# Kernel optimization log

Measured on AMD Instinct MI355X. Metric: run time of the kernel, lower is better.

The kernel has to match this reference:

```python
import jax, jax.numpy as jnp
import numpy as np

H = 8                 # num_heads
SCALE = 25.0          # self.scale
SIM_THRESH = 0.75
CONF_SIM_THRESH = 0.99


def _l2n(x):
    return x / jnp.linalg.norm(x, axis=-1, keepdims=True)


def setup_inputs() -> dict:
    key = jax.random.key(0)
    ks = jax.random.split(key, 10)
    B, N1, N2, C = 1, 512, 2048, 1024
    s = 0.02
    return {
        'x_cls': jax.random.normal(ks[0], (B, N2, C), jnp.float32),
        'x_reg': jax.random.normal(ks[1], (B, N2, C), jnp.float32),
        'cls_score': jax.random.uniform(ks[2], (N2,), dtype=jnp.float32),
        'fg_score': jax.random.uniform(ks[3], (N2,), dtype=jnp.float32),
        'W_q_cls': jax.random.normal(ks[4], (C, C), jnp.float32) * s,
        'W_kv_cls': jax.random.normal(ks[5], (C, 2 * C), jnp.float32) * s,
        'W_q_reg': jax.random.normal(ks[6], (C, C), jnp.float32) * s,
        'W_kv_reg': jax.random.normal(ks[7], (C, 2 * C), jnp.float32) * s,
        'W_lin': jax.random.normal(ks[8], (2 * C, 2 * C), jnp.float32) * s,
        'b_lin': jnp.zeros((2 * C,), jnp.float32),
        'W_lin_reg': jax.random.normal(ks[9], (2 * C, 2 * C), jnp.float32) * s,
        'b_lin_reg': jnp.zeros((2 * C,), jnp.float32),
        'local_preds_num': 512,
    }


def _forward(x_cls, x_reg, cls_score, fg_score, W_q_cls, W_kv_cls, W_q_reg, W_kv_reg,
             W_lin, b_lin, W_lin_reg, b_lin_reg, N1):
    B, N2, C = x_cls.shape
    hd = C // H
    # QKV projections (torch Linear with bias=False; weights stored [in,out])
    q_cls = (x_cls[:, :N1] @ W_q_cls).reshape(B, N1, H, hd).transpose(0, 2, 1, 3)   # [B,H,N1,hd]
    kv = (x_cls @ W_kv_cls).reshape(B, N2, 2, H, hd).transpose(2, 0, 3, 1, 4)
    k_cls, v_cls = kv[0], kv[1]                                                      # [B,H,N2,hd]
    q_reg = (x_reg[:, :N1] @ W_q_reg).reshape(B, N1, H, hd).transpose(0, 2, 1, 3)
    kv = (x_reg @ W_kv_reg).reshape(B, N2, 2, H, hd).transpose(2, 0, 3, 1, 4)
    k_reg, v_reg = kv[0], kv[1]
    # L2 normalization of q, k and of v for raw similarity
    q_cls, k_cls = _l2n(q_cls), _l2n(k_cls)
    q_reg, k_reg = _l2n(q_reg), _l2n(k_reg)
    v_cls_n, v_reg_n = _l2n(v_cls), _l2n(v_reg)
    # per-key score broadcast over [1,H,N1,N2] (use_mask=False path)
    cs = cls_score.reshape(1, 1, 1, N2)
    # raw value-value similarity
    attn_cls_raw = jnp.einsum('bhqd,bhkd->bhqk', v_cls_n[:, :, :N1], v_cls_n)        # [B,H,N1,N2]
    attn_reg_raw = jnp.einsum('bhqd,bhkd->bhqk', v_reg_n[:, :, :N1], v_reg_n)
    # blended softmax attention (attn_drop=0 -> identity)
    attn_cls = jax.nn.softmax(jnp.einsum('bhqd,bhkd->bhqk', q_cls, k_cls) * SCALE * cs, axis=-1)
    attn_reg = jax.nn.softmax(jnp.einsum('bhqd,bhkd->bhqk', q_reg, k_reg) * SCALE, axis=-1)
    attn = (attn_cls + attn_reg) * 0.5
    # attended features + original local values, then output linears
    x = jnp.einsum('bhqk,bhkd->bhqd', attn, v_cls).transpose(0, 2, 1, 3).reshape(B, N1, C)
    x_ori = v_cls[:, :, :N1].transpose(0, 2, 1, 3).reshape(B, N1, C)
    out_cls = jnp.concatenate([x, x_ori], axis=-1) @ W_lin + b_lin                   # [B,N1,2C]
    xr = jnp.einsum('bhqk,bhkd->bhqd', attn, v_reg).transpose(0, 2, 1, 3).reshape(B, N1, C)
    xr_ori = v_reg[:, :, :N1].transpose(0, 2, 1, 3).reshape(B, N1, C)
    out_reg = jnp.concatenate([xr, xr_ori], axis=-1) @ W_lin_reg + b_lin_reg         # reconf=True
    # ave branch: similarity-masked renormalized second-round averaging (batch 0)
    sim_mask = (attn_cls_raw.sum(axis=1)[0] / H > SIM_THRESH).astype(x_cls.dtype)    # [N1,N2]
    obj_mask = (attn_reg_raw.sum(axis=1)[0] / H > CONF_SIM_THRESH).astype(x_cls.dtype)
    sim_round2 = jax.nn.softmax(attn.sum(axis=1)[0] / H, axis=-1)
    sim_round2 = sim_mask * sim_round2
    sim_round2 = sim_round2 / sim_round2.sum(axis=-1, keepdims=True)
    obj_w = obj_mask * sim_round2
    obj_w = obj_w / obj_w.sum(axis=-1, keepdims=True)
    support_cls = v_cls.transpose(0, 2, 1, 3).reshape(B, N2, C)[0]                   # [N2,C]
    support_reg = v_reg.transpose(0, 2, 1, 3).reshape(B, N2, C)[0]
    cls_feature = jnp.concatenate([sim_round2 @ support_cls, out_cls[0]], axis=-1)   # [N1,3C]
    reg_feature = jnp.concatenate([obj_w @ support_reg, out_reg[0]], axis=-1)        # [N1,3C]
    return cls_feature, reg_feature


def reference(x_cls, x_reg, cls_score, fg_score, W_q_cls, W_kv_cls, W_q_reg, W_kv_reg,
              W_lin, b_lin, W_lin_reg, b_lin_reg, local_preds_num):
    return _forward(x_cls, x_reg, cls_score, fg_score, W_q_cls, W_kv_cls, W_q_reg,
                    W_kv_reg, W_lin, b_lin, W_lin_reg, b_lin_reg, local_preds_num)
```

## Files before the change

kernel.cpp:

```cpp
#include <hip/hip_runtime.h>

constexpr int kN1 = 512;
constexpr int kN2 = 2048;
constexpr int kC  = 1024;
constexpr int kHD = 128;
constexpr int kC2 = 2048;
constexpr int kC3 = 3072;

typedef _Float16 half8 __attribute__((ext_vector_type(8)));
typedef _Float16 half4v __attribute__((ext_vector_type(4)));
typedef float f32x4 __attribute__((ext_vector_type(4)));

#define GLD16(gptr, lptr) \
    __builtin_amdgcn_global_load_lds((const __attribute__((address_space(1))) void*)(gptr), \
                                     (__attribute__((address_space(3))) void*)(lptr), 16, 0, 0)

#define WAIT_VM8   0x0F78
#define WAIT_VM0   0x0F70
#define WAIT_LGKM0 0xC07F

struct GD {
    const _Float16* A; const _Float16* B; void* C;
    const float* colScale;
    long sAh, sAg, sBh, sBg, sSplit, sCh, sCg;
    int lda, ldb, ldc, K, SK, hmask, hshift;
    int ahx, outHalf, csMode, nx, ny;
    float alpha;
};

__global__ __launch_bounds__(256)
void hgemm2(GD d0, GD d1, int zSplit)
{
    const bool second = (int)blockIdx.z >= zSplit;
    const GD& d = second ? d1 : d0;
    const int bz = second ? (int)blockIdx.z - zSplit : (int)blockIdx.z;
    if ((int)blockIdx.x >= d.nx || (int)blockIdx.y >= d.ny) return;

    __shared__ uint4 smem[4096];
    char* smembase = (char*)smem;
    const int tid = threadIdx.x;
    const int w = tid >> 6, l = tid & 63;
    const int m0 = blockIdx.y << 7, n0 = blockIdx.x << 7;
    const int wm = (w >> 1) << 6, wn = (w & 1) << 6;
    const int kq = l >> 4, lm = l & 15;

    const int zz = bz / d.SK, s = bz - zz * d.SK;
    const int h = d.ahx ? (int)blockIdx.x : (zz & d.hmask);
    const int g = d.ahx ? zz : (zz >> d.hshift);
    const _Float16* A = d.A + (long)h * d.sAh + (long)g * d.sAg;
    const _Float16* B = d.B + (long)h * d.sBh + (long)g * d.sBg;
    const long Coff = (long)s * d.sSplit + (long)h * d.sCh + (long)g * d.sCg;
    const int kper = d.K / d.SK, kbeg = s * kper;
    const int nIter = kper >> 6;

    const int skq = w >> 1;
    const int sr0 = (w & 1) << 6;
    const _Float16* gA = A + (long)(m0 + sr0 + l) * d.lda + skq * 8 + kbeg;
    const _Float16* gB = B + (long)(n0 + sr0 + l) * d.ldb + skq * 8 + kbeg;
    const int soff = skq * 2048 + (sr0 + l) * 16;

    auto stage = [&](int it, int b) {
        char* dst = smembase + b * 32768;
        const int k0 = it << 6;
        GLD16(gA + k0,      dst + soff);
        GLD16(gA + k0 + 16, dst + soff + 4096);
        GLD16(gA + k0 + 32, dst + soff + 8192);
        GLD16(gA + k0 + 48, dst + soff + 12288);
        GLD16(gB + k0,      dst + 16384 + soff);
        GLD16(gB + k0 + 16, dst + 16384 + soff + 4096);
        GLD16(gB + k0 + 32, dst + 16384 + soff + 8192);
        GLD16(gB + k0 + 48, dst + 16384 + soff + 12288);
    };

    f32x4 acc[4][4] = {};
    stage(0, 0);

    for (int it = 0; it < nIter; ++it) {
        const int cur = it & 1;
        if (it + 1 < nIter) {
            stage(it + 1, cur ^ 1);
            __builtin_amdgcn_s_waitcnt(WAIT_VM8);
        } else {
            __builtin_amdgcn_s_waitcnt(WAIT_VM0);
        }
        __builtin_amdgcn_s_barrier();
        const char* cbase = smembase + cur * 32768;
        #pragma unroll
        for (int ks = 0; ks < 2; ++ks) {
            half8 af[4], bfr[4];
            const char* pa = cbase + ks * 8192 + kq * 2048 + (wm + lm) * 16;
            const char* pb = cbase + 16384 + ks * 8192 + kq * 2048 + (wn + lm) * 16;
            #pragma unroll
            for (int i = 0; i < 4; ++i) {
                af[i]  = *(const half8*)(pa + i * 256);
                bfr[i] = *(const half8*)(pb + i * 256);
            }
            #pragma unroll
            for (int mi = 0; mi < 4; ++mi)
                #pragma unroll
                for (int ni = 0; ni < 4; ++ni)
                    acc[mi][ni] = __builtin_amdgcn_mfma_f32_16x16x32_f16(af[mi], bfr[ni], acc[mi][ni], 0, 0, 0);
        }
        __builtin_amdgcn_s_waitcnt(WAIT_LGKM0);
        __builtin_amdgcn_s_barrier();
    }

    const int rbase = m0 + wm + kq * 4;
    #pragma unroll
    for (int mi = 0; mi < 4; ++mi) {
        #pragma unroll
        for (int ni = 0; ni < 4; ++ni) {
            const int col = n0 + wn + ni * 16 + lm;
            float cs = d.alpha;
            if (d.csMode == 1 || (d.csMode == 2 && g == 0)) cs *= d.colScale[col];
            #pragma unroll
            for (int r = 0; r < 4; ++r) {
                const long row = rbase + mi * 16 + r;
                const float v = acc[mi][ni][r] * cs;
                const long off = Coff + row * d.ldc + col;
                if (d.outHalf) ((_Float16*)d.C)[off] = (_Float16)v;
                else           ((float*)d.C)[off] = v;
            }
        }
    }
}

static GD mkgd(const _Float16* A, const _Float16* B, void* C, const float* cscale,
               long sAh, long sAg, long sBh, long sBg, long sSplit, long sCh, long sCg,
               int lda, int ldb, int ldc, int K, int SK, int hmask, int hshift,
               int ahx, int outHalf, int csMode, int nx, int ny, float alpha)
{
    GD d; d.A=A; d.B=B; d.C=C; d.colScale=cscale;
    d.sAh=sAh; d.sAg=sAg; d.sBh=sBh; d.sBg=sBg; d.sSplit=sSplit; d.sCh=sCh; d.sCg=sCg;
    d.lda=lda; d.ldb=ldb; d.ldc=ldc; d.K=K; d.SK=SK; d.hmask=hmask; d.hshift=hshift;
    d.ahx=ahx; d.outHalf=outHalf; d.csMode=csMode; d.nx=nx; d.ny=ny; d.alpha=alpha;
    return d;
}

__global__ __launch_bounds__(256)
void cast_f2h(const float* __restrict__ s0, const float* __restrict__ s1,
              _Float16* __restrict__ d, int n4)
{
    const int i = blockIdx.x * 256 + threadIdx.x;
    const float* s = blockIdx.y ? s1 : s0;
    const float4 v = ((const float4*)s)[i];
    half4v o;
    o.x = (_Float16)v.x; o.y = (_Float16)v.y; o.z = (_Float16)v.z; o.w = (_Float16)v.w;
    ((half4v*)(d + (size_t)blockIdx.y * n4 * 4))[i] = o;
}

__global__ __launch_bounds__(256)
void prep_transpose(const float* __restrict__ Wq_c, const float* __restrict__ Wq_r,
                    const float* __restrict__ Wkv_c, const float* __restrict__ Wkv_r,
                    const float* __restrict__ Wl_c, const float* __restrict__ Wl_r,
                    _Float16* __restrict__ WqT, _Float16* __restrict__ WkvT,
                    _Float16* __restrict__ WlinT)
{
    __shared__ float t[32][33];
    const int z = blockIdx.z;
    const float* src; _Float16* dst; int ldsrc, lddst, nx, ky;
    switch (z) {
        case 0: src=Wq_c;  dst=WqT;            ldsrc=1024; lddst=1024; nx=32; ky=32; break;
        case 1: src=Wq_r;  dst=WqT+1048576;    ldsrc=1024; lddst=1024; nx=32; ky=32; break;
        case 2: src=Wkv_c; dst=WkvT;           ldsrc=2048; lddst=1024; nx=64; ky=32; break;
        case 3: src=Wkv_r; dst=WkvT+2097152;   ldsrc=2048; lddst=1024; nx=64; ky=32; break;
        case 4: src=Wl_c;  dst=WlinT;          ldsrc=2048; lddst=2048; nx=64; ky=64; break;
        default:src=Wl_r;  dst=WlinT+4194304;  ldsrc=2048; lddst=2048; nx=64; ky=64; break;
    }
    if ((int)blockIdx.x >= nx || (int)blockIdx.y >= ky) return;
    const int n0 = blockIdx.x << 5, k0 = blockIdx.y << 5;
    const int tx = threadIdx.x & 31, ty = threadIdx.x >> 5;
    #pragma unroll
    for (int j = ty; j < 32; j += 8)
        t[j][tx] = src[(size_t)(k0 + j) * ldsrc + n0 + tx];
    __syncthreads();
    #pragma unroll
    for (int j = ty; j < 32; j += 8)
        dst[(size_t)(n0 + j) * lddst + k0 + tx] = (_Float16)t[tx][j];
}

__global__ __launch_bounds__(256)
void phase3(const _Float16* __restrict__ qpart, const _Float16* __restrict__ kvh,
            _Float16* __restrict__ qn, _Float16* __restrict__ kn,
            _Float16* __restrict__ vn, _Float16* __restrict__ x_ori,
            _Float16* __restrict__ vT)
{
    __shared__ float t[32][33];
    const int b = blockIdx.x;
    if (b < 2048) {
        const int vid = b * 4 + (threadIdx.x >> 6);
        const int lane = threadIdx.x & 63;
        const int g = vid >> 12, rr = vid & 4095, row = rr >> 3, hh = rr & 7;
        const size_t o = (size_t)g * 524288 + (size_t)row * 1024 + hh * 128 + lane * 2;
        float a = 0.f, bb = 0.f;
        #pragma unroll
        for (int s = 0; s < 4; ++s) {
            a  += (float)qpart[(size_t)s * 1048576 + o];
            bb += (float)qpart[(size_t)s * 1048576 + o + 1];
        }
        float ss = a * a + bb * bb;
        #pragma unroll
        for (int d = 32; d > 0; d >>= 1) ss += __shfl_xor(ss, d, 64);
        const float inv = rsqrtf(ss);
        qn[o] = (_Float16)(a * inv); qn[o + 1] = (_Float16)(bb * inv);
    } else if (b < 18432) {
        const int vid = (b - 2048) * 4 + (threadIdx.x >> 6);
        const int lane = threadIdx.x & 63;
        const int half_ = vid >> 15;
        const int r15 = vid & 32767;
        const int g = r15 >> 14, rr = r15 & 16383, row = rr >> 3, hh = rr & 7;
        const size_t so = (size_t)g * 4194304 + (size_t)row * 2048
                        + half_ * 1024 + hh * 128 + lane * 2;
        const float a = (float)kvh[so], bb = (float)kvh[so + 1];
        float ss = a * a + bb * bb;
        #pragma unroll
        for (int d = 32; d > 0; d >>= 1) ss += __shfl_xor(ss, d, 64);
        const float inv = rsqrtf(ss);
        const size_t dofs = (size_t)g * 2097152 + (size_t)row * 1024 + hh * 128 + lane * 2;
        _Float16* dp = (half_ ? vn : kn) + dofs;
        dp[0] = (_Float16)(a * inv); dp[1] = (_Float16)(bb * inv);
        if (half_ == 1 && row < 512) {
            _Float16* xo = x_ori + (size_t)g * 524288 + (size_t)row * 1024 + hh * 128 + lane * 2;
            xo[0] = (_Float16)a; xo[1] = (_Float16)bb;
        }
    } else {
        const int vb = b - 18432;
        const int g = vb >> 11, r = vb & 2047;
        const int n0 = (r & 31) << 5, k0 = (r >> 5) << 5;
        const int tx = threadIdx.x & 31, ty = threadIdx.x >> 5;
        const _Float16* s0 = kvh + (size_t)g * 4194304 + 1024;
        #pragma unroll
        for (int j = ty; j < 32; j += 8)
            t[j][tx] = (float)s0[(size_t)(k0 + j) * 2048 + n0 + tx];
        __syncthreads();
        _Float16* d = vT + (size_t)g * 2097152;
        #pragma unroll
        for (int j = ty; j < 32; j += 8)
            d[(size_t)(n0 + j) * 2048 + k0 + tx] = (_Float16)t[tx][j];
    }
}

template<int OP>
__device__ __forceinline__ float bred(float v, float* lds)
{
    #pragma unroll
    for (int o = 32; o > 0; o >>= 1) {
        const float u = __shfl_xor(v, o, 64);
        v = OP ? fmaxf(v, u) : v + u;
    }
    __syncthreads();
    if ((threadIdx.x & 63) == 0) lds[threadIdx.x >> 6] = v;
    __syncthreads();
    return OP ? fmaxf(fmaxf(lds[0], lds[1]), fmaxf(lds[2], lds[3]))
              : lds[0] + lds[1] + lds[2] + lds[3];
}

__global__ __launch_bounds__(256)
void sb2_kernel(const _Float16* __restrict__ S16, const float* __restrict__ simPart,
                _Float16* __restrict__ attn,
                _Float16* __restrict__ wc, _Float16* __restrict__ wr)
{
    __shared__ float lds[4];
    const int q = blockIdx.x, t = threadIdx.x;
    float asum[8] = {};
    for (int hh = 0; hh < 8; ++hh) {
        const size_t rb = (size_t)(hh * 512 + q) * 2048;
        float vc[8], vr[8];
        float mc = -1e30f, mr = -1e30f;
        #pragma unroll
        for (int j = 0; j < 8; ++j) {
            vc[j] = (float)S16[rb + t + 256 * j];
            vr[j] = (float)S16[8388608 + rb + t + 256 * j];
            mc = fmaxf(mc, vc[j]); mr = fmaxf(mr, vr[j]);
        }
        mc = bred<1>(mc, lds);
        mr = bred<1>(mr, lds);
        float sc = 0.f, sr = 0.f;
        #pragma unroll
        for (int j = 0; j < 8; ++j) {
            vc[j] = expf(vc[j] - mc); sc += vc[j];
            vr[j] = expf(vr[j] - mr); sr += vr[j];
        }
        sc = bred<0>(sc, lds);
        sr = bred<0>(sr, lds);
        const float ic = 0.5f / sc, ir = 0.5f / sr;
        #pragma unroll
        for (int j = 0; j < 8; ++j) {
            const float a = vc[j] * ic + vr[j] * ir;
            attn[rb + t + 256 * j] = (_Float16)a;
            asum[j] += a;
        }
    }
    float mx = -1e30f;
    #pragma unroll
    for (int j = 0; j < 8; ++j) { asum[j] *= 0.125f; mx = fmaxf(mx, asum[j]); }
    mx = bred<1>(mx, lds);
    float em[8], emo[8];
    float s1 = 0.f, s2 = 0.f;
    const size_t qb = (size_t)q * 2048;
    #pragma unroll
    for (int j = 0; j < 8; ++j) {
        const size_t o = qb + t + 256 * j;
        const float sim = simPart[o] + simPart[2097152 + o];
        const float reg = simPart[1048576 + o] + simPart[3145728 + o];
        const float e = expf(asum[j] - mx);
        const float m  = sim > 0.75f ? 1.f : 0.f;
        const float mo = reg > 0.99f ? 1.f : 0.f;
        em[j] = e * m; emo[j] = e * m * mo;
        s1 += em[j]; s2 += emo[j];
    }
    s1 = bred<0>(s1, lds);
    s2 = bred<0>(s2, lds);
    const float i1 = 1.f / s1, i2 = 1.f / s2;
    #pragma unroll
    for (int j = 0; j < 8; ++j) {
        wc[qb + t + 256 * j] = (_Float16)(em[j] * i1);
        wr[qb + t + 256 * j] = (_Float16)(emo[j] * i2);
    }
}

__global__ __launch_bounds__(256)
void build_xcat(const float* __restrict__ xcatPart, const _Float16* __restrict__ x_ori,
                _Float16* __restrict__ xcat)
{
    const int idx = blockIdx.x * 256 + threadIdx.x;
    const int j = idx & 2047;
    const int n = (idx >> 11) & 511;
    const int g = idx >> 20;
    _Float16 v;
    if (j < 1024) {
        float a = 0.f;
        #pragma unroll
        for (int s = 0; s < 4; ++s)
            a += xcatPart[(size_t)s * 1048576 + (size_t)g * 524288 + n * 1024 + j];
        v = (_Float16)a;
    } else {
        v = x_ori[(size_t)g * 524288 + (size_t)n * 1024 + (j - 1024)];
    }
    xcat[idx] = v;
}

__global__ __launch_bounds__(256)
void finalize(const float* __restrict__ avePart, const float* __restrict__ outPart,
              const float* __restrict__ b_lin, const float* __restrict__ b_lin_reg,
              float* __restrict__ out)
{
    const int idx = blockIdx.x * 256 + threadIdx.x;
    const int c = idx % 3072;
    const int r = (idx / 3072) & 511;
    const int g = idx / (3072 * 512);
    float v;
    if (c < 1024) {
        v = 0.f;
        #pragma unroll
        for (int s = 0; s < 4; ++s)
            v += avePart[(size_t)s * 1048576 + (size_t)g * 524288 + r * 1024 + c];
    } else {
        const int cc = c - 1024;
        v = (g ? b_lin_reg : b_lin)[cc];
        #pragma unroll
        for (int s = 0; s < 4; ++s)
            v += outPart[(size_t)s * 2097152 + (size_t)g * 1048576 + r * 2048 + cc];
    }
    out[idx] = v;
}

extern "C" void kernel_launch(void* const* d_in, const int* in_sizes, int n_in,
                              void* d_out, int out_size, void* d_ws, size_t ws_size,
                              hipStream_t stream)
{
    const float* x_cls     = (const float*)d_in[0];
    const float* x_reg     = (const float*)d_in[1];
    const float* cls_score = (const float*)d_in[2];
    const float* W_q_cls   = (const float*)d_in[4];
    const float* W_kv_cls  = (const float*)d_in[5];
    const float* W_q_reg   = (const float*)d_in[6];
    const float* W_kv_reg  = (const float*)d_in[7];
    const float* W_lin     = (const float*)d_in[8];
    const float* b_lin     = (const float*)d_in[9];
    const float* W_lin_reg = (const float*)d_in[10];
    const float* b_lin_reg = (const float*)d_in[11];
    float* out = (float*)d_out;

    if (ws_size < (size_t)124 * 1048576) return;

    char* W = (char*)d_ws;
    auto at = [&](size_t mb) { return (void*)(W + mb * 1048576); };
    _Float16* WlinT   = (_Float16*)at(0);
    _Float16* vT      = (_Float16*)at(16);
    _Float16* x_ori   = (_Float16*)at(24);
    _Float16* w_c     = (_Float16*)at(26);
    _Float16* w_r     = (_Float16*)at(28);
    _Float16* qn      = (_Float16*)at(30);
    _Float16* kvh     = (_Float16*)at(32);
    float*    simPart = (float*)at(32);
    _Float16* qpart16 = (_Float16*)at(48);
    _Float16* xcat16  = (_Float16*)at(48);
    _Float16* xbf     = (_Float16*)at(56);
    _Float16* WqT     = (_Float16*)at(64);
    _Float16* WkvT    = (_Float16*)at(68);
    _Float16* kn      = (_Float16*)at(76);
    _Float16* vn      = (_Float16*)at(84);
    _Float16* attn_h  = (_Float16*)at(76);
    float*    outPart = (float*)at(56);
    _Float16* S16     = (_Float16*)at(92);
    float*    xcatPart= (float*)at(92);
    float*    avePart = (float*)at(108);

    cast_f2h<<<dim3(2048, 2), 256, 0, stream>>>(x_cls, x_reg, xbf, 524288);
    prep_transpose<<<dim3(64, 64, 6), 256, 0, stream>>>(
        W_q_cls, W_q_reg, W_kv_cls, W_kv_reg, W_lin, W_lin_reg, WqT, WkvT, WlinT);

    {
        GD kv = mkgd(xbf, WkvT, kvh, nullptr,
                     0, 2097152, 0, 2097152, 0, 0, 4194304,
                     1024, 1024, 2048, 1024, 1, 0, 0, 0, 1, 0, 16, 16, 1.f);
        GD q  = mkgd(xbf, WqT, qpart16, nullptr,
                     0, 2097152, 0, 1048576, 1048576, 0, 524288,
                     1024, 1024, 1024, 1024, 4, 0, 0, 0, 1, 0, 8, 4, 1.f);
        hgemm2<<<dim3(16, 16, 10), 256, 0, stream>>>(kv, q, 2);
    }

    phase3<<<22528, 256, 0, stream>>>(qpart16, kvh, qn, kn, vn, x_ori, vT);

    {
        GD vs = mkgd(vn, vn, simPart, nullptr,
                     0, 2097152, 0, 2097152, 2097152, 0, 1048576,
                     1024, 1024, 2048, 1024, 2, 0, 0, 0, 0, 0, 16, 4, 0.125f);
        GD sc = mkgd(qn, kn, S16, cls_score,
                     128, 524288, 128, 2097152, 0, 1048576, 8388608,
                     1024, 1024, 2048, 128, 1, 7, 3, 0, 1, 2, 16, 4, 25.f);
        hgemm2<<<dim3(16, 4, 20), 256, 0, stream>>>(vs, sc, 4);
    }

    sb2_kernel<<<512, 256, 0, stream>>>(S16, simPart, attn_h, w_c, w_r);

    {
        GD av = mkgd(attn_h, vT, xcatPart, nullptr,
                     1048576, 0, 0, 2097152, 1048576, 0, 524288,
                     2048, 2048, 1024, 2048, 4, 0, 0, 1, 0, 0, 8, 4, 1.f);
        GD ae = mkgd(w_c, vT, avePart, nullptr,
                     0, 1048576, 0, 2097152, 1048576, 0, 524288,
                     2048, 2048, 1024, 2048, 4, 0, 0, 0, 0, 0, 8, 4, 1.f);
        hgemm2<<<dim3(8, 4, 16), 256, 0, stream>>>(av, ae, 8);
    }

    build_xcat<<<8192, 256, 0, stream>>>(xcatPart, x_ori, xcat16);

    {
        GD ol = mkgd(xcat16, WlinT, outPart, nullptr,
                     0, 1048576, 0, 4194304, 2097152, 0, 1048576,
                     2048, 2048, 2048, 2048, 4, 0, 0, 0, 0, 0, 16, 4, 1.f);
        hgemm2<<<dim3(16, 4, 8), 256, 0, stream>>>(ol, ol, 8);
    }

    finalize<<<12288, 256, 0, stream>>>(avePart, outPart, b_lin, b_lin_reg, out);
}
```

Baseline: 337.4 us.

## Rework GEMM into 256x128 tiles with 5-stage K32 LDS pipeline and rebalanced split-K

Replaces the double-buffered 128x128, K64 GEMM with a 512-thread 256x128 tile kernel. It uses a 5-slot ring of K32 LDS stages with three stages in flight, aiming to hide global-load latency better and raise reuse per block. The Q projection drops split-K (so phase3 reads Q directly), and the KV projection moves to split-K 2, with phase3 summing the two partials. All launch grids and workspace offsets change to match. Larger tiles mean fewer blocks for some GEMMs and more register/LDS pressure per block.

```diff
diff --git a/kernel.cpp b/kernel.cpp
--- a/kernel.cpp
+++ b/kernel.cpp
@@ -1,11 +1,4 @@
 #include <hip/hip_runtime.h>
-
-constexpr int kN1 = 512;
-constexpr int kN2 = 2048;
-constexpr int kC  = 1024;
-constexpr int kHD = 128;
-constexpr int kC2 = 2048;
-constexpr int kC3 = 3072;
 
 typedef _Float16 half8 __attribute__((ext_vector_type(8)));
 typedef _Float16 half4v __attribute__((ext_vector_type(4)));
@@ -15,7 +8,8 @@
     __builtin_amdgcn_global_load_lds((const __attribute__((address_space(1))) void*)(gptr), \
                                      (__attribute__((address_space(3))) void*)(lptr), 16, 0, 0)
 
-#define WAIT_VM8   0x0F78
+#define WAIT_VM6   0x0F76
+#define WAIT_VM3   0x0F73
 #define WAIT_VM0   0x0F70
 #define WAIT_LGKM0 0xC07F
 
@@ -28,19 +22,19 @@
     float alpha;
 };
 
-__global__ __launch_bounds__(256)
-void hgemm2(GD d0, GD d1, int zSplit)
+__global__ __launch_bounds__(512, 2)
+void hgemm3(GD d0, GD d1, int zSplit)
 {
     const bool second = (int)blockIdx.z >= zSplit;
     const GD& d = second ? d1 : d0;
     const int bz = second ? (int)blockIdx.z - zSplit : (int)blockIdx.z;
     if ((int)blockIdx.x >= d.nx || (int)blockIdx.y >= d.ny) return;
 
-    __shared__ uint4 smem[4096];
-    char* smembase = (char*)smem;
+    __shared__ uint4 smem[7680];
+    char* sb = (char*)smem;
     const int tid = threadIdx.x;
     const int w = tid >> 6, l = tid & 63;
-    const int m0 = blockIdx.y << 7, n0 = blockIdx.x << 7;
+    const int m0 = blockIdx.y << 8, n0 = blockIdx.x << 7;
     const int wm = (w >> 1) << 6, wn = (w & 1) << 6;
     const int kq = l >> 4, lm = l & 15;
 
@@ -51,57 +45,49 @@
     const _Float16* B = d.B + (long)h * d.sBh + (long)g * d.sBg;
     const long Coff = (long)s * d.sSplit + (long)h * d.sCh + (long)g * d.sCg;
     const int kper = d.K / d.SK, kbeg = s * kper;
-    const int nIter = kper >> 6;
-
-    const int skq = w >> 1;
-    const int sr0 = (w & 1) << 6;
-    const _Float16* gA = A + (long)(m0 + sr0 + l) * d.lda + skq * 8 + kbeg;
-    const _Float16* gB = B + (long)(n0 + sr0 + l) * d.ldb + skq * 8 + kbeg;
-    const int soff = skq * 2048 + (sr0 + l) * 16;
-
-    auto stage = [&](int it, int b) {
-        char* dst = smembase + b * 32768;
-        const int k0 = it << 6;
-        GLD16(gA + k0,      dst + soff);
-        GLD16(gA + k0 + 16, dst + soff + 4096);
-        GLD16(gA + k0 + 32, dst + soff + 8192);
-        GLD16(gA + k0 + 48, dst + soff + 12288);
-        GLD16(gB + k0,      dst + 16384 + soff);
-        GLD16(gB + k0 + 16, dst + 16384 + soff + 4096);
-        GLD16(gB + k0 + 32, dst + 16384 + soff + 8192);
-        GLD16(gB + k0 + 48, dst + 16384 + soff + 12288);
+    const int NT = kper >> 5;
+
+    const int rA = ((w & 3) << 6) + l, cA = w >> 2;
+    const int rB = ((w & 1) << 6) + l, cB = w >> 1;
+    const _Float16* gA = A + (long)(m0 + rA) * d.lda + kbeg;
+    const _Float16* gB = B + (long)(n0 + rB) * d.ldb + kbeg;
+    const int lo = w * 1024 + l * 16;
+
+    auto stage = [&](int t) {
+        char* dst = sb + (t % 5) * 24576;
+        GLD16(gA + t * 32 + cA * 8,       dst + lo);
+        GLD16(gA + t * 32 + (cA + 2) * 8, dst + 8192 + lo);
+        GLD16(gB + t * 32 + cB * 8,       dst + 16384 + lo);
     };
 
     f32x4 acc[4][4] = {};
-    stage(0, 0);
-
-    for (int it = 0; it < nIter; ++it) {
-        const int cur = it & 1;
-        if (it + 1 < nIter) {
-            stage(it + 1, cur ^ 1);
-            __builtin_amdgcn_s_waitcnt(WAIT_VM8);
-        } else {
-            __builtin_amdgcn_s_waitcnt(WAIT_VM0);
-        }
-        __builtin_amdgcn_s_barrier();
-        const char* cbase = smembase + cur * 32768;
-        #pragma unroll
-        for (int ks = 0; ks < 2; ++ks) {
-            half8 af[4], bfr[4];
-            const char* pa = cbase + ks * 8192 + kq * 2048 + (wm + lm) * 16;
-            const char* pb = cbase + 16384 + ks * 8192 + kq * 2048 + (wn + lm) * 16;
+    stage(0);
+    if (NT > 1) stage(1);
+    if (NT > 2) stage(2);
+    if (NT > 2)      __builtin_amdgcn_s_waitcnt(WAIT_VM6);
+    else if (NT > 1) __builtin_amdgcn_s_waitcnt(WAIT_VM3);
+    else             __builtin_amdgcn_s_waitcnt(WAIT_VM0);
+    __builtin_amdgcn_s_barrier();
+
+    for (int t = 0; t < NT; ++t) {
+        const char* cb = sb + (t % 5) * 24576;
+        half8 af[4], bfr[4];
+        const char* pa = cb + kq * 4096 + (wm + lm) * 16;
+        const char* pb = cb + 16384 + kq * 2048 + (wn + lm) * 16;
+        #pragma unroll
+        for (int i = 0; i < 4; ++i) {
+            af[i]  = *(const half8*)(pa + i * 256);
+            bfr[i] = *(const half8*)(pb + i * 256);
+        }
+        #pragma unroll
+        for (int mi = 0; mi < 4; ++mi)
             #pragma unroll
-            for (int i = 0; i < 4; ++i) {
-                af[i]  = *(const half8*)(pa + i * 256);
-                bfr[i] = *(const half8*)(pb + i * 256);
-            }
-            #pragma unroll
-            for (int mi = 0; mi < 4; ++mi)
-                #pragma unroll
-                for (int ni = 0; ni < 4; ++ni)
-                    acc[mi][ni] = __builtin_amdgcn_mfma_f32_16x16x32_f16(af[mi], bfr[ni], acc[mi][ni], 0, 0, 0);
-        }
+            for (int ni = 0; ni < 4; ++ni)
+                acc[mi][ni] = __builtin_amdgcn_mfma_f32_16x16x32_f16(af[mi], bfr[ni], acc[mi][ni], 0, 0, 0);
         __builtin_amdgcn_s_waitcnt(WAIT_LGKM0);
+        if (t + 3 < NT) { stage(t + 3); __builtin_amdgcn_s_waitcnt(WAIT_VM6); }
+        else if (t + 2 < NT) __builtin_amdgcn_s_waitcnt(WAIT_VM3);
+        else if (t + 1 < NT) __builtin_amdgcn_s_waitcnt(WAIT_VM0);
         __builtin_amdgcn_s_barrier();
     }
 
@@ -180,7 +166,7 @@
 }
 
 __global__ __launch_bounds__(256)
-void phase3(const _Float16* __restrict__ qpart, const _Float16* __restrict__ kvh,
+void phase3(const _Float16* __restrict__ qh, const _Float16* __restrict__ kvh,
             _Float16* __restrict__ qn, _Float16* __restrict__ kn,
             _Float16* __restrict__ vn, _Float16* __restrict__ x_ori,
             _Float16* __restrict__ vT)
@@ -192,12 +178,7 @@
         const int lane = threadIdx.x & 63;
         const int g = vid >> 12, rr = vid & 4095, row = rr >> 3, hh = rr & 7;
         const size_t o = (size_t)g * 524288 + (size_t)row * 1024 + hh * 128 + lane * 2;
-        float a = 0.f, bb = 0.f;
-        #pragma unroll
-        for (int s = 0; s < 4; ++s) {
-            a  += (float)qpart[(size_t)s * 1048576 + o];
-            bb += (float)qpart[(size_t)s * 1048576 + o + 1];
-        }
+        const float a = (float)qh[o], bb = (float)qh[o + 1];
         float ss = a * a + bb * bb;
         #pragma unroll
         for (int d = 32; d > 0; d >>= 1) ss += __shfl_xor(ss, d, 64);
@@ -211,7 +192,8 @@
         const int g = r15 >> 14, rr = r15 & 16383, row = rr >> 3, hh = rr & 7;
         const size_t so = (size_t)g * 4194304 + (size_t)row * 2048
                         + half_ * 1024 + hh * 128 + lane * 2;
-        const float a = (float)kvh[so], bb = (float)kvh[so + 1];
+        const float a  = (float)kvh[so] + (float)kvh[8388608 + so];
+        const float bb = (float)kvh[so + 1] + (float)kvh[8388608 + so + 1];
         float ss = a * a + bb * bb;
         #pragma unroll
         for (int d = 32; d > 0; d >>= 1) ss += __shfl_xor(ss, d, 64);
@@ -230,8 +212,10 @@
         const int tx = threadIdx.x & 31, ty = threadIdx.x >> 5;
         const _Float16* s0 = kvh + (size_t)g * 4194304 + 1024;
         #pragma unroll
-        for (int j = ty; j < 32; j += 8)
-            t[j][tx] = (float)s0[(size_t)(k0 + j) * 2048 + n0 + tx];
+        for (int j = ty; j < 32; j += 8) {
+            const size_t idx = (size_t)(k0 + j) * 2048 + n0 + tx;
+            t[j][tx] = (float)s0[idx] + (float)s0[8388608 + idx];
+        }
         __syncthreads();
         _Float16* d = vT + (size_t)g * 2097152;
         #pragma unroll
@@ -394,43 +378,43 @@
     _Float16* qn      = (_Float16*)at(30);
     _Float16* kvh     = (_Float16*)at(32);
     float*    simPart = (float*)at(32);
-    _Float16* qpart16 = (_Float16*)at(48);
-    _Float16* xcat16  = (_Float16*)at(48);
-    _Float16* xbf     = (_Float16*)at(56);
-    _Float16* WqT     = (_Float16*)at(64);
-    _Float16* WkvT    = (_Float16*)at(68);
-    _Float16* kn      = (_Float16*)at(76);
-    _Float16* vn      = (_Float16*)at(84);
-    _Float16* attn_h  = (_Float16*)at(76);
-    float*    outPart = (float*)at(56);
-    _Float16* S16     = (_Float16*)at(92);
-    float*    xcatPart= (float*)at(92);
-    float*    avePart = (float*)at(108);
+    float*    outPart = (float*)at(32);
+    _Float16* qh      = (_Float16*)at(64);
+    _Float16* WqT     = (_Float16*)at(66);
+    _Float16* WkvT    = (_Float16*)at(70);
+    _Float16* kn      = (_Float16*)at(66);
+    _Float16* vn      = (_Float16*)at(74);
+    _Float16* attn_h  = (_Float16*)at(66);
+    _Float16* xbf     = (_Float16*)at(82);
+    _Float16* xcat16  = (_Float16*)at(82);
+    _Float16* S16     = (_Float16*)at(90);
+    float*    xcatPart= (float*)at(90);
+    float*    avePart = (float*)at(106);
 
     cast_f2h<<<dim3(2048, 2), 256, 0, stream>>>(x_cls, x_reg, xbf, 524288);
     prep_transpose<<<dim3(64, 64, 6), 256, 0, stream>>>(
         W_q_cls, W_q_reg, W_kv_cls, W_kv_reg, W_lin, W_lin_reg, WqT, WkvT, WlinT);
 
     {
+        GD q  = mkgd(xbf, WqT, qh, nullptr,
+                     0, 2097152, 0, 1048576, 0, 0, 524288,
+                     1024, 1024, 1024, 1024, 1, 0, 0, 0, 1, 0, 8, 2, 1.f);
         GD kv = mkgd(xbf, WkvT, kvh, nullptr,
-                     0, 2097152, 0, 2097152, 0, 0, 4194304,
-                     1024, 1024, 2048, 1024, 1, 0, 0, 0, 1, 0, 16, 16, 1.f);
-        GD q  = mkgd(xbf, WqT, qpart16, nullptr,
-                     0, 2097152, 0, 1048576, 1048576, 0, 524288,
-                     1024, 1024, 1024, 1024, 4, 0, 0, 0, 1, 0, 8, 4, 1.f);
-        hgemm2<<<dim3(16, 16, 10), 256, 0, stream>>>(kv, q, 2);
-    }
-
-    phase3<<<22528, 256, 0, stream>>>(qpart16, kvh, qn, kn, vn, x_ori, vT);
+                     0, 2097152, 0, 2097152, 8388608, 0, 4194304,
+                     1024, 1024, 2048, 1024, 2, 0, 0, 0, 1, 0, 16, 8, 1.f);
+        hgemm3<<<dim3(16, 8, 6), 512, 0, stream>>>(q, kv, 2);
+    }
+
+    phase3<<<22528, 256, 0, stream>>>(qh, kvh, qn, kn, vn, x_ori, vT);
 
     {
         GD vs = mkgd(vn, vn, simPart, nullptr,
                      0, 2097152, 0, 2097152, 2097152, 0, 1048576,
-                     1024, 1024, 2048, 1024, 2, 0, 0, 0, 0, 0, 16, 4, 0.125f);
+                     1024, 1024, 2048, 1024, 2, 0, 0, 0, 0, 0, 16, 2, 0.125f);
         GD sc = mkgd(qn, kn, S16, cls_score,
                      128, 524288, 128, 2097152, 0, 1048576, 8388608,
-                     1024, 1024, 2048, 128, 1, 7, 3, 0, 1, 2, 16, 4, 25.f);
-        hgemm2<<<dim3(16, 4, 20), 256, 0, stream>>>(vs, sc, 4);
+                     1024, 1024, 2048, 128, 1, 7, 3, 0, 1, 2, 16, 2, 25.f);
+        hgemm3<<<dim3(16, 2, 20), 512, 0, stream>>>(vs, sc, 4);
     }
 
     sb2_kernel<<<512, 256, 0, stream>>>(S16, simPart, attn_h, w_c, w_r);
@@ -438,11 +422,11 @@
     {
         GD av = mkgd(attn_h, vT, xcatPart, nullptr,
                      1048576, 0, 0, 2097152, 1048576, 0, 524288,
-                     2048, 2048, 1024, 2048, 4, 0, 0, 1, 0, 0, 8, 4, 1.f);
+                     2048, 2048, 1024, 2048, 4, 0, 0, 1, 0, 0, 8, 2, 1.f);
         GD ae = mkgd(w_c, vT, avePart, nullptr,
                      0, 1048576, 0, 2097152, 1048576, 0, 524288,
-                     2048, 2048, 1024, 2048, 4, 0, 0, 0, 0, 0, 8, 4, 1.f);
-        hgemm2<<<dim3(8, 4, 16), 256, 0, stream>>>(av, ae, 8);
+                     2048, 2048, 1024, 2048, 4, 0, 0, 0, 0, 0, 8, 2, 1.f);
+        hgemm3<<<dim3(8, 2, 16), 512, 0, stream>>>(av, ae, 8);
     }
 
     build_xcat<<<8192, 256, 0, stream>>>(xcatPart, x_ori, xcat16);
@@ -450,8 +434,8 @@
     {
         GD ol = mkgd(xcat16, WlinT, outPart, nullptr,
                      0, 1048576, 0, 4194304, 2097152, 0, 1048576,
-                     2048, 2048, 2048, 2048, 4, 0, 0, 0, 0, 0, 16, 4, 1.f);
-        hgemm2<<<dim3(16, 4, 8), 256, 0, stream>>>(ol, ol, 8);
+                     2048, 2048, 2048, 2048, 4, 0, 0, 0, 0, 0, 16, 2, 1.f);
+        hgemm3<<<dim3(16, 2, 8), 512, 0, stream>>>(ol, ol, 8);
     }
 
     finalize<<<12288, 256, 0, stream>>>(avePart, outPart, b_lin, b_lin_reg, out);
```

Result: slower. 344.7 us (+2.2%).
